# Performance work log

Measured on AMD Instinct MI355X. Metric: run time of the kernel, lower is better.

Reference implementation:

```python
import jax, jax.numpy as jnp
import numpy as np

B, S, D = 2, 2048, 4096
H, G, HD = 32, 8, 128          # num_heads, num_kv_groups, head_dim
GROUP = H // G                  # group_size = 4
SCALE = HD ** -0.5


def setup_inputs() -> dict:
    key = jax.random.key(0)
    ks = jax.random.split(key, 6)
    x = jax.random.normal(ks[0], (B, S, D), dtype=jnp.float32)
    # Linear weights stored as [in, out] (y = x @ W), no bias, 0.02 init scale
    Wq = jax.random.normal(ks[1], (D, H * HD), dtype=jnp.float32) * 0.02
    Wk = jax.random.normal(ks[2], (D, G * HD), dtype=jnp.float32) * 0.02
    Wv = jax.random.normal(ks[3], (D, G * HD), dtype=jnp.float32) * 0.02
    Wo = jax.random.normal(ks[4], (H * HD, D), dtype=jnp.float32) * 0.02
    # RoPE tables: [S, HD], duplicated-half layout (rotate-half convention)
    inv_freq = 1.0 / (10000.0 ** (jnp.arange(0, HD, 2, dtype=jnp.float32) / HD))
    angles = jnp.arange(S, dtype=jnp.float32)[:, None] * inv_freq[None, :]  # [S, HD/2]
    angles = jnp.concatenate([angles, angles], axis=-1)                      # [S, HD]
    cos = jnp.cos(angles)
    sin = jnp.sin(angles)
    # causal mask: True = masked (strict upper triangle)
    mask = jnp.triu(jnp.ones((S, S), dtype=bool), k=1)
    return {"x": x, "Wq": Wq, "Wk": Wk, "Wv": Wv, "Wo": Wo,
            "cos": cos, "sin": sin, "mask": mask, "start_pos": 0}


def _rope(t, cos, sin, offset):
    # t: [B, h, S, HD]; cos/sin: [S_total, HD]
    n = t.shape[2]
    c = jax.lax.dynamic_slice_in_dim(cos, offset, n, axis=0)  # [n, HD]
    s = jax.lax.dynamic_slice_in_dim(sin, offset, n, axis=0)
    t1, t2 = t[..., : HD // 2], t[..., HD // 2:]
    rotated = jnp.concatenate([-t2, t1], axis=-1)
    return t * c[None, None] + rotated * s[None, None]


def reference(x, Wq, Wk, Wv, Wo, cos, sin, mask, start_pos):
    # projections
    q = (x @ Wq).reshape(B, S, H, HD).transpose(0, 2, 1, 3)   # [B,H,S,HD]
    k = (x @ Wk).reshape(B, S, G, HD).transpose(0, 2, 1, 3)   # [B,G,S,HD]
    v = (x @ Wv).reshape(B, S, G, HD).transpose(0, 2, 1, 3)   # [B,G,S,HD]
    # RoPE (no cache: prev_len = 0)
    q = _rope(q, cos, sin, start_pos) * SCALE
    k = _rope(k, cos, sin, start_pos)
    # GQA: expand kv groups to full heads (repeat_interleave along head dim)
    k_r = jnp.repeat(k, GROUP, axis=1)                         # [B,H,S,HD]
    v_r = jnp.repeat(v, GROUP, axis=1)
    scores = jnp.einsum('bhqd,bhkd->bhqk', q, k_r)             # [B,H,S,S]
    scores = jnp.where(mask[None, None], -jnp.inf, scores)
    w = jax.nn.softmax(scores, axis=-1)
    ctx = jnp.einsum('bhqk,bhkd->bhqd', w, v_r)                # [B,H,S,HD]
    ctx = ctx.transpose(0, 2, 1, 3).reshape(B, S, H * HD)
    out = ctx @ Wo                                             # [B,S,D]
    return out
```

## Files before the change

### kernel.cpp

```cpp
#include <hip/hip_runtime.h>
#include <hip/hip_bf16.h>
#include <math.h>

#define B_ 2
#define S_ 2048
#define D_ 4096
#define H_ 32
#define G_ 8
#define HD_ 128
#define GROUP_ 4
#define KVSTR_ (2 * G_ * HD_)
#define SCALE_ 0.08838834764831845f

typedef short bfv8 __attribute__((ext_vector_type(8)));
typedef float f32x4 __attribute__((ext_vector_type(4)));

__device__ __forceinline__ f32x4 mfma16(bfv8 a, bfv8 b, f32x4 c) {
  return __builtin_amdgcn_mfma_f32_16x16x32_bf16(a, b, c, 0, 0, 0);
}

__device__ __forceinline__ ushort f2bf_bits(float f) {
  __hip_bfloat16 h = __float2bfloat16(f);
  return *reinterpret_cast<ushort*>(&h);
}

__device__ __forceinline__ void gload16(const short* g, short* l) {
  __builtin_amdgcn_global_load_lds(
      (const __attribute__((address_space(1))) void*)g,
      (__attribute__((address_space(3))) void*)l, 16, 0, 0);
}

__global__ __launch_bounds__(256) void k_cvt(const float* __restrict__ in,
                                             ushort* __restrict__ out, int n4) {
  int i = blockIdx.x * 256 + threadIdx.x;
  if (i >= n4) return;
  float4 v = *(const float4*)(in + (size_t)i * 4);
  ushort4 o;
  o.x = f2bf_bits(v.x); o.y = f2bf_bits(v.y); o.z = f2bf_bits(v.z); o.w = f2bf_bits(v.w);
  *(ushort4*)(out + (size_t)i * 4) = o;
}

__global__ __launch_bounds__(256) void k_transpose(const float* __restrict__ in,
                                                   ushort* __restrict__ out,
                                                   int R, int C) {
  __shared__ ushort tile[32][36];
  int bc = blockIdx.x * 32;
  int br = blockIdx.y * 32;
  int t = threadIdx.x;
  int rr = t >> 3;
  int c4 = (t & 7) * 4;
  float4 v = *(const float4*)(in + (size_t)(br + rr) * C + bc + c4);
  tile[rr][c4 + 0] = f2bf_bits(v.x);
  tile[rr][c4 + 1] = f2bf_bits(v.y);
  tile[rr][c4 + 2] = f2bf_bits(v.z);
  tile[rr][c4 + 3] = f2bf_bits(v.w);
  __syncthreads();
  int cc = t >> 3;
  int r4 = (t & 7) * 4;
  ushort4 o;
  o.x = tile[r4 + 0][cc];
  o.y = tile[r4 + 1][cc];
  o.z = tile[r4 + 2][cc];
  o.w = tile[r4 + 3][cc];
  *(ushort4*)(out + (size_t)(bc + cc) * R + br + r4) = o;
}

__global__ __launch_bounds__(256) void k_transpose_v(const ushort* __restrict__ v,
                                                     ushort* __restrict__ vt,
                                                     int hstride, int hoff) {
  __shared__ ushort tile[32][33];
  int bg = blockIdx.z;
  int b = bg / G_, g = bg % G_;
  int s0 = blockIdx.y * 32;
  int h0 = blockIdx.x * 32;
  int tx = threadIdx.x, ty = threadIdx.y;
  const ushort* src = v + (size_t)b * S_ * hstride + (size_t)(hoff + g) * HD_;
  ushort* dst = vt + (size_t)(b * G_ + g) * HD_ * S_;
  for (int ii = 0; ii < 4; ii++) {
    int i = ty + ii * 8;
    tile[i][tx] = src[(size_t)(s0 + i) * hstride + h0 + tx];
  }
  __syncthreads();
  for (int ii = 0; ii < 4; ii++) {
    int i = ty + ii * 8;
    dst[(size_t)(h0 + i) * S_ + s0 + tx] = tile[tx][i];
  }
}

__global__ __launch_bounds__(256) void k_rope(__hip_bfloat16* __restrict__ t,
                                              const float* __restrict__ cosb,
                                              const float* __restrict__ sinb,
                                              int hstride, int nlaunch, float scale) {
  int item = blockIdx.x * 4 + (threadIdx.x >> 6);
  int head = item % nlaunch;
  int row = item / nlaunch;
  int s = row & (S_ - 1);
  int l = threadIdx.x & 63;
  size_t base = (size_t)row * hstride * HD_ + (size_t)head * HD_;
  float x1 = __bfloat162float(t[base + l]);
  float x2 = __bfloat162float(t[base + 64 + l]);
  float c1 = cosb[s * HD_ + l];
  float sn1 = sinb[s * HD_ + l];
  float c2 = cosb[s * HD_ + 64 + l];
  float sn2 = sinb[s * HD_ + 64 + l];
  t[base + l] = __float2bfloat16((x1 * c1 - x2 * sn1) * scale);
  t[base + 64 + l] = __float2bfloat16((x2 * c2 + x1 * sn2) * scale);
}

template <typename OT>
__global__ __launch_bounds__(256) void k_gemm_bt(const __hip_bfloat16* __restrict__ Ab,
                                                 const __hip_bfloat16* __restrict__ BTb,
                                                 OT* __restrict__ Cb,
                                                 int M, int N, int K) {
  __shared__ short sA[128 * 32];
  __shared__ short sB[128 * 32];
  int t = threadIdx.x;
  int w = t >> 6;
  int l = t & 63;
  int row0 = blockIdx.y * 128;
  int col0 = blockIdx.x * 128;
  int wr = (w >> 1) * 64;
  int wc = (w & 1) * 64;
  int fr = l & 15;
  int fq = l >> 4;
  int fo = fq * 8;
  int srow = l >> 2;
  int schk = (l & 3) * 8;

  const short* gA = (const short*)Ab;
  const short* gB = (const short*)BTb;

  f32x4 acc[4][4];
#pragma unroll
  for (int m = 0; m < 4; m++)
#pragma unroll
    for (int n = 0; n < 4; n++) acc[m][n] = (f32x4){0.f, 0.f, 0.f, 0.f};

  for (int k0 = 0; k0 < K; k0 += 32) {
    __syncthreads();
#pragma unroll
    for (int j = 0; j < 2; j++) {
      int r = w * 32 + j * 16;
      gload16(gA + (size_t)(row0 + r + srow) * K + k0 + schk, &sA[r * 32]);
      gload16(gB + (size_t)(col0 + r + srow) * K + k0 + schk, &sB[r * 32]);
    }
    __syncthreads();
    bfv8 af[4], bff[4];
#pragma unroll
    for (int m = 0; m < 4; m++) af[m] = *(const bfv8*)(sA + (wr + m * 16 + fr) * 32 + fo);
#pragma unroll
    for (int n = 0; n < 4; n++) bff[n] = *(const bfv8*)(sB + (wc + n * 16 + fr) * 32 + fo);
#pragma unroll
    for (int m = 0; m < 4; m++)
#pragma unroll
      for (int n = 0; n < 4; n++)
        acc[m][n] = mfma16(af[m], bff[n], acc[m][n]);
  }
#pragma unroll
  for (int m = 0; m < 4; m++)
#pragma unroll
    for (int n = 0; n < 4; n++)
#pragma unroll
      for (int j = 0; j < 4; j++) {
        int r = row0 + wr + m * 16 + fq * 4 + j;
        int c = col0 + wc + n * 16 + fr;
        if constexpr (__is_same(OT, float)) {
          Cb[(size_t)r * N + c] = acc[m][n][j];
        } else {
          Cb[(size_t)r * N + c] = __float2bfloat16(acc[m][n][j]);
        }
      }
}

template <typename OT>
__global__ __launch_bounds__(512, 2) void k_gemm256(const __hip_bfloat16* __restrict__ Ab,
                                                    const __hip_bfloat16* __restrict__ BTb,
                                                    OT* __restrict__ Cb,
                                                    int M, int N, int K) {
  __shared__ short sA[2][2][8192];
  __shared__ short sB[2][2][8192];
  int tid = threadIdx.x;
  int wid = tid >> 6;
  int l = tid & 63;
  int wr = (wid >> 2) * 128;
  int wc = (wid & 3) * 64;
  int fr = l & 15, fq = l >> 4;
  int cswz = (fq ^ ((fr >> 1) & 3)) * 8;
  int row0 = blockIdx.y * 256, col0 = blockIdx.x * 256;
  int sr = l >> 2;
  int schunk = ((l & 3) ^ (((wid * 16 + sr) >> 1) & 3)) * 8;
  const short* gA = (const short*)Ab;
  const short* gB = (const short*)BTb;

  f32x4 acc[8][4];
#pragma unroll
  for (int m = 0; m < 8; m++)
#pragma unroll
    for (int n = 0; n < 4; n++) acc[m][n] = (f32x4){0.f, 0.f, 0.f, 0.f};

#define STAGE256(buf, kh, isB, kt)                                                   \
  {                                                                                  \
    const short* g_ = (isB) ? gB : gA;                                               \
    int b0_ = (isB) ? col0 : row0;                                                   \
    short* s_ = (isB) ? &sB[buf][kh][0] : &sA[buf][kh][0];                           \
    int k0_ = (kt) * 64 + (kh) * 32;                                                 \
    _Pragma("unroll")                                                                \
    for (int i_ = 0; i_ < 2; i_++) {                                                 \
      int r_ = i_ * 128 + wid * 16 + sr;                                             \
      gload16(g_ + (size_t)(b0_ + r_) * K + k0_ + schunk,                            \
              s_ + (i_ * 128 + wid * 16) * 32);                                      \
    }                                                                                \
  }

  bfv8 bf[4];
#define COMPUTE256(cur, kh, mg, loadB)                                               \
  {                                                                                  \
    if (loadB) {                                                                     \
      _Pragma("unroll")                                                              \
      for (int n_ = 0; n_ < 4; n_++)                                                 \
        bf[n_] = *(const bfv8*)&sB[cur][kh][(wc + n_ * 16 + fr) * 32 + cswz];        \
    }                                                                                \
    bfv8 af_[4];                                                                     \
    _Pragma("unroll")                                                                \
    for (int j_ = 0; j_ < 4; j_++)                                                   \
      af_[j_] = *(const bfv8*)&sA[cur][kh][(wr + ((mg) * 4 + j_) * 16 + fr) * 32 + cswz]; \
    __builtin_amdgcn_s_setprio(1);                                                   \
    _Pragma("unroll")                                                                \
    for (int j_ = 0; j_ < 4; j_++)                                                   \
      _Pragma("unroll")                                                              \
      for (int n_ = 0; n_ < 4; n_++)                                                 \
        acc[(mg) * 4 + j_][n_] = mfma16(af_[j_], bf[n_], acc[(mg) * 4 + j_][n_]);    \
    __builtin_amdgcn_s_setprio(0);                                                   \
  }

  int NT = K / 64;
  STAGE256(0, 0, false, 0);
  STAGE256(0, 0, true, 0);
  STAGE256(0, 1, false, 0);
  STAGE256(0, 1, true, 0);

  for (int t = 0; t < NT - 1; t++) {
    int cur = t & 1, nxt = cur ^ 1;
    asm volatile("s_waitcnt vmcnt(4)" ::: "memory");
    __builtin_amdgcn_s_barrier();
    STAGE256(nxt, 0, false, t + 1);
    COMPUTE256(cur, 0, 0, true);
    STAGE256(nxt, 0, true, t + 1);
    COMPUTE256(cur, 0, 1, false);
    asm volatile("s_waitcnt vmcnt(4)" ::: "memory");
    __builtin_amdgcn_s_barrier();
    STAGE256(nxt, 1, false, t + 1);
    COMPUTE256(cur, 1, 0, true);
    STAGE256(nxt, 1, true, t + 1);
    COMPUTE256(cur, 1, 1, false);
  }
  {
    int cur = (NT - 1) & 1;
    asm volatile("s_waitcnt vmcnt(4)" ::: "memory");
    __builtin_amdgcn_s_barrier();
    COMPUTE256(cur, 0, 0, true);
    COMPUTE256(cur, 0, 1, false);
    asm volatile("s_waitcnt vmcnt(0)" ::: "memory");
    __builtin_amdgcn_s_barrier();
    COMPUTE256(cur, 1, 0, true);
    COMPUTE256(cur, 1, 1, false);
  }
#undef STAGE256
#undef COMPUTE256

#pragma unroll
  for (int m = 0; m < 8; m++)
#pragma unroll
    for (int n = 0; n < 4; n++)
#pragma unroll
      for (int j = 0; j < 4; j++) {
        int r = row0 + wr + m * 16 + fq * 4 + j;
        int c = col0 + wc + n * 16 + fr;
        if constexpr (__is_same(OT, float)) {
          Cb[(size_t)r * N + c] = acc[m][n][j];
        } else {
          Cb[(size_t)r * N + c] = __float2bfloat16(acc[m][n][j]);
        }
      }
}

#define PSTR 68
__global__ __launch_bounds__(512) void k_attn2(const __hip_bfloat16* __restrict__ Qb,
                                               const __hip_bfloat16* __restrict__ KVb,
                                               const __hip_bfloat16* __restrict__ VTb,
                                               __hip_bfloat16* __restrict__ ctx) {
  __shared__ short sK[64 * 128];
  __shared__ short sV[128 * 64];
  __shared__ short sP[8][16 * PSTR];

  const int nQB = S_ / 128;
  int blk = blockIdx.x;
  int qb = (nQB - 1) - (blk % nQB);
  int bh = blk / nQB;
  int h = bh % H_;
  int b = bh / H_;
  int g = h / GROUP_;
  int q0 = qb * 128;

  int t = threadIdx.x;
  int wid = t >> 6;
  int l = t & 63;
  int fr = l & 15, fq = l >> 4, fo = fq * 8;
  int wq0 = q0 + wid * 16;

  const short* qp = (const short*)Qb + (size_t)b * S_ * H_ * HD_ + (size_t)h * HD_;
  const short* kp = (const short*)KVb + (size_t)b * S_ * KVSTR_ + (size_t)g * HD_;
  const short* vp = (const short*)VTb + (size_t)(b * G_ + g) * HD_ * S_;

  bfv8 qf[4];
#pragma unroll
  for (int c = 0; c < 4; c++)
    qf[c] = *(const bfv8*)(qp + (size_t)(wq0 + fr) * (H_ * HD_) + c * 32 + fo);

  f32x4 acc[8];
#pragma unroll
  for (int n = 0; n < 8; n++) acc[n] = (f32x4){0.f, 0.f, 0.f, 0.f};
  float m[4], ll[4];
#pragma unroll
  for (int j = 0; j < 4; j++) { m[j] = -INFINITY; ll[j] = 0.f; }

  int krow_i = l >> 4;
  int kchk = l & 15;
  int vrow_i = l >> 3;
  int vchk = l & 7;

  int nkt = 2 * qb + 2;
  for (int kt = 0; kt < nkt; kt++) {
    int k0 = kt * 64;
#pragma unroll
    for (int j = 0; j < 2; j++) {
      int base = wid * 8 + j * 4;
      int r = base + krow_i;
      gload16(kp + (size_t)(k0 + r) * KVSTR_ + ((kchk ^ (r & 7)) * 8), &sK[base * 128]);
    }
#pragma unroll
    for (int j = 0; j < 2; j++) {
      int base = wid * 16 + j * 8;
      int r = base + vrow_i;
      gload16(vp + (size_t)r * S_ + k0 + ((vchk ^ (r & 7)) * 8), &sV[base * 64]);
    }
    __syncthreads();

    f32x4 sf[4];
#pragma unroll
    for (int ks = 0; ks < 4; ks++) {
      sf[ks] = (f32x4){0.f, 0.f, 0.f, 0.f};
      int row = ks * 16 + fr;
      int rx = row & 7;
#pragma unroll
      for (int c = 0; c < 4; c++) {
        bfv8 kf = *(const bfv8*)&sK[row * 128 + (((c * 4 + fq) ^ rx) * 8)];
        sf[ks] = mfma16(qf[c], kf, sf[ks]);
      }
    }

    float p[4][4], sc[4], red[4];
#pragma unroll
    for (int j = 0; j < 4; j++) {
      int q = wq0 + fq * 4 + j;
#pragma unroll
      for (int ks = 0; ks < 4; ks++)
        if (k0 + ks * 16 + fr > q) sf[ks][j] = -INFINITY;
      red[j] = fmaxf(fmaxf(sf[0][j], sf[1][j]), fmaxf(sf[2][j], sf[3][j]));
    }
#pragma unroll
    for (int off = 1; off < 16; off <<= 1)
#pragma unroll
      for (int j = 0; j < 4; j++)
        red[j] = fmaxf(red[j], __shfl_xor(red[j], off, 64));
#pragma unroll
    for (int j = 0; j < 4; j++) {
      float nm = fmaxf(m[j], red[j]);
      sc[j] = __expf(m[j] - nm);
      m[j] = nm;
#pragma unroll
      for (int ks = 0; ks < 4; ks++) p[ks][j] = __expf(sf[ks][j] - nm);
      red[j] = (p[0][j] + p[1][j]) + (p[2][j] + p[3][j]);
    }
#pragma unroll
    for (int off = 1; off < 16; off <<= 1)
#pragma unroll
      for (int j = 0; j < 4; j++)
        red[j] += __shfl_xor(red[j], off, 64);
#pragma unroll
    for (int j = 0; j < 4; j++) {
      ll[j] = ll[j] * sc[j] + red[j];
#pragma unroll
      for (int n = 0; n < 8; n++) acc[n][j] *= sc[j];
#pragma unroll
      for (int ks = 0; ks < 4; ks++)
        sP[wid][(fq * 4 + j) * PSTR + ks * 16 + fr] = f2bf_bits(p[ks][j]);
    }

    bfv8 pa0 = *(const bfv8*)&sP[wid][fr * PSTR + fo];
    bfv8 pa1 = *(const bfv8*)&sP[wid][fr * PSTR + 32 + fo];
#pragma unroll
    for (int n = 0; n < 8; n++) {
      int row = n * 16 + fr;
      int rx = row & 7;
      bfv8 vf0 = *(const bfv8*)&sV[row * 64 + ((fq ^ rx) * 8)];
      bfv8 vf1 = *(const bfv8*)&sV[row * 64 + (((4 + fq) ^ rx) * 8)];
      acc[n] = mfma16(pa0, vf0, acc[n]);
      acc[n] = mfma16(pa1, vf1, acc[n]);
    }
    __syncthreads();
  }

#pragma unroll
  for (int n = 0; n < 8; n++)
#pragma unroll
    for (int j = 0; j < 4; j++) {
      int q = wq0 + fq * 4 + j;
      float o = acc[n][j] / ll[j];
      ctx[(size_t)(b * S_ + q) * (H_ * HD_) + h * HD_ + n * 16 + fr] = __float2bfloat16(o);
    }
}

extern "C" void kernel_launch(void* const* d_in, const int* in_sizes, int n_in,
                              void* d_out, int out_size, void* d_ws, size_t ws_size,
                              hipStream_t stream) {
  (void)in_sizes; (void)n_in; (void)out_size; (void)ws_size;
  const float* x    = (const float*)d_in[0];
  const float* Wq   = (const float*)d_in[1];
  const float* Wk   = (const float*)d_in[2];
  const float* Wv   = (const float*)d_in[3];
  const float* Wo   = (const float*)d_in[4];
  const float* cosb = (const float*)d_in[5];
  const float* sinb = (const float*)d_in[6];

  char* ws = (char*)d_ws;
  __hip_bfloat16* xb  = (__hip_bfloat16*)(ws + 0);
  __hip_bfloat16* WqT = (__hip_bfloat16*)(ws + 33554432);
  __hip_bfloat16* WkT = (__hip_bfloat16*)(ws + 67108864);
  __hip_bfloat16* WvT = (__hip_bfloat16*)(ws + 75497472);
  __hip_bfloat16* Qb  = (__hip_bfloat16*)(ws + 83886080);
  __hip_bfloat16* KVb = (__hip_bfloat16*)(ws + 117440512);
  __hip_bfloat16* VTb = (__hip_bfloat16*)(ws + 134217728);
  __hip_bfloat16* Cx  = xb;

  k_cvt<<<(B_ * S_ * D_ / 4 + 255) / 256, 256, 0, stream>>>(x, (ushort*)xb, B_ * S_ * D_ / 4);
  k_transpose<<<dim3(128, 128), 256, 0, stream>>>(Wq, (ushort*)WqT, 4096, 4096);
  k_transpose<<<dim3(32, 128), 256, 0, stream>>>(Wk, (ushort*)WkT, 4096, 1024);
  k_transpose<<<dim3(32, 128), 256, 0, stream>>>(Wv, (ushort*)WvT, 4096, 1024);

  k_gemm256<__hip_bfloat16><<<dim3(16, 16), 512, 0, stream>>>(xb, WqT, Qb, 4096, 4096, 4096);
  k_gemm_bt<__hip_bfloat16><<<dim3(16, 32), 256, 0, stream>>>(xb, WkT, KVb, 4096, 2048, 4096);

  k_transpose<<<dim3(128, 128), 256, 0, stream>>>(Wo, (ushort*)WqT, 4096, 4096);

  k_rope<<<4096 * 32 / 4, 256, 0, stream>>>(Qb, cosb, sinb, 32, 32, SCALE_);
  k_rope<<<4096 * 8 / 4, 256, 0, stream>>>((__hip_bfloat16*)KVb, cosb, sinb, 16, 8, 1.0f);

  k_transpose_v<<<dim3(4, 64, 16), dim3(32, 8), 0, stream>>>((const ushort*)KVb, (ushort*)VTb,
                                                             KVSTR_, G_);

  k_attn2<<<B_ * H_ * (S_ / 128), 512, 0, stream>>>(Qb, KVb, VTb, Cx);

  k_gemm256<float><<<dim3(16, 16), 512, 0, stream>>>(Cx, WqT, (float*)d_out, 4096, 4096, 4096);
}
```

Measured before the change: 737.9 us.

## Overlap next K/V tile loads with attention compute using split waits

Restructures the attention loop so the next K tile is prefetched into shared memory during the P·V stage and the next V tile after it, using vmcnt waits and raw barriers in place of full __syncthreads. The aim is to hide global-to-LDS load latency behind the MFMA and softmax work within a single-buffered scheme. The approach relies on gload16 being counted by vmcnt and on carefully placed barriers, so misordering could cause races on sK/sV.

```diff
diff --git a/kernel.cpp b/kernel.cpp
--- a/kernel.cpp
+++ b/kernel.cpp
@@ -285,7 +285,7 @@
 }
 
 #define PSTR 68
-__global__ __launch_bounds__(512) void k_attn2(const __hip_bfloat16* __restrict__ Qb,
+__global__ __launch_bounds__(512) void k_attn5(const __hip_bfloat16* __restrict__ Qb,
                                                const __hip_bfloat16* __restrict__ KVb,
                                                const __hip_bfloat16* __restrict__ VTb,
                                                __hip_bfloat16* __restrict__ ctx) {
@@ -329,22 +329,30 @@
   int vrow_i = l >> 3;
   int vchk = l & 7;
 
+#define STAGE_K(k0s)                                                                 \
+  _Pragma("unroll")                                                                  \
+  for (int j = 0; j < 2; j++) {                                                      \
+    int base = wid * 8 + j * 4;                                                      \
+    int r = base + krow_i;                                                           \
+    gload16(kp + (size_t)((k0s) + r) * KVSTR_ + ((kchk ^ (r & 7)) * 8),              \
+            &sK[base * 128]);                                                        \
+  }
+#define STAGE_V(k0s)                                                                 \
+  _Pragma("unroll")                                                                  \
+  for (int j = 0; j < 2; j++) {                                                      \
+    int base = wid * 16 + j * 8;                                                     \
+    int r = base + vrow_i;                                                           \
+    gload16(vp + (size_t)r * S_ + (k0s) + ((vchk ^ (r & 7)) * 8), &sV[base * 64]);   \
+  }
+
   int nkt = 2 * qb + 2;
+  STAGE_K(0);
+  STAGE_V(0);
+
   for (int kt = 0; kt < nkt; kt++) {
     int k0 = kt * 64;
-#pragma unroll
-    for (int j = 0; j < 2; j++) {
-      int base = wid * 8 + j * 4;
-      int r = base + krow_i;
-      gload16(kp + (size_t)(k0 + r) * KVSTR_ + ((kchk ^ (r & 7)) * 8), &sK[base * 128]);
-    }
-#pragma unroll
-    for (int j = 0; j < 2; j++) {
-      int base = wid * 16 + j * 8;
-      int r = base + vrow_i;
-      gload16(vp + (size_t)r * S_ + k0 + ((vchk ^ (r & 7)) * 8), &sV[base * 64]);
-    }
-    __syncthreads();
+    asm volatile("s_waitcnt vmcnt(2)" ::: "memory");
+    __builtin_amdgcn_s_barrier();
 
     f32x4 sf[4];
 #pragma unroll
@@ -396,6 +404,10 @@
       for (int ks = 0; ks < 4; ks++)
         sP[wid][(fq * 4 + j) * PSTR + ks * 16 + fr] = f2bf_bits(p[ks][j]);
     }
+
+    asm volatile("s_waitcnt vmcnt(0)" ::: "memory");
+    __builtin_amdgcn_s_barrier();
+    if (kt + 1 < nkt) STAGE_K(k0 + 64);
 
     bfv8 pa0 = *(const bfv8*)&sP[wid][fr * PSTR + fo];
     bfv8 pa1 = *(const bfv8*)&sP[wid][fr * PSTR + 32 + fo];
@@ -408,8 +420,14 @@
       acc[n] = mfma16(pa0, vf0, acc[n]);
       acc[n] = mfma16(pa1, vf1, acc[n]);
     }
-    __syncthreads();
-  }
+
+    if (kt + 1 < nkt) {
+      __builtin_amdgcn_s_barrier();
+      STAGE_V(k0 + 64);
+    }
+  }
+#undef STAGE_K
+#undef STAGE_V
 
 #pragma unroll
   for (int n = 0; n < 8; n++)
@@ -459,7 +477,7 @@
   k_transpose_v<<<dim3(4, 64, 16), dim3(32, 8), 0, stream>>>((const ushort*)KVb, (ushort*)VTb,
                                                              KVSTR_, G_);
 
-  k_attn2<<<B_ * H_ * (S_ / 128), 512, 0, stream>>>(Qb, KVb, VTb, Cx);
+  k_attn5<<<B_ * H_ * (S_ / 128), 512, 0, stream>>>(Qb, KVb, VTb, Cx);
 
   k_gemm256<float><<<dim3(16, 16), 512, 0, stream>>>(Cx, WqT, (float*)d_out, 4096, 4096, 4096);
 }
```

Measured after the change: 715.5 us. -3.0%, faster.
